# Performance work log

Measured on AMD Instinct MI355X. Metric: run time of the kernel, lower is better.

Reference implementation:

```python
import jax, jax.numpy as jnp
import numpy as np

ACT_BIT = 8
W_BIT = 8
EPS = 1e-8


def ste_round(x):
    # straight-through round (matches torch STE quant autograd)
    return x + jax.lax.stop_gradient(jnp.round(x) - x)


def quant_act(x):
    """Per-tensor symmetric 8-bit activation quantization (HAWQ QuantAct)."""
    n = 2 ** (ACT_BIT - 1) - 1  # 127
    x_max = jax.lax.stop_gradient(jnp.max(jnp.abs(x)))
    scale = jnp.maximum(x_max, EPS) / n
    x_int = jnp.clip(ste_round(x / scale), -n - 1, n)
    return x_int * scale, scale


def quant_linear(x_q, act_scale, weight, bias):
    """Per-channel symmetric 8-bit weight quant + integer matmul + fused dequant."""
    n = 2 ** (W_BIT - 1) - 1  # 127
    w_max = jax.lax.stop_gradient(jnp.max(jnp.abs(weight), axis=1, keepdims=True))  # [out,1]
    w_scale = jnp.maximum(w_max, EPS) / n                                            # [out,1]
    w_int = jnp.clip(ste_round(weight / w_scale), -n - 1, n)                         # [out,in]
    bias_scale = w_scale[:, 0] * act_scale                                           # [out]
    b_int = ste_round(bias / bias_scale)                                             # [out]
    x_int = x_q / act_scale                                   # integer-valued float, [..., in]
    out_int = jnp.einsum('...i,oi->...o', x_int, w_int)       # int8-domain GEMM in float
    return (out_int + b_int) * bias_scale                     # fused dequant


def setup_inputs() -> dict:
    key = jax.random.key(0)
    k1, k2, k3 = jax.random.split(key, 3)
    L, B, Q, D, O = 6, 8, 1024, 1024, 1024
    hs = jax.random.normal(k1, (L, B, Q, D), dtype=jnp.float32)
    weight = jax.random.normal(k2, (O, D), dtype=jnp.float32) * 0.02
    bias = jax.random.normal(k3, (O,), dtype=jnp.float32) * 0.02
    return {"hs": hs, "weight": weight, "bias": bias}


def reference(hs, weight, bias):
    x_q, act_scale = quant_act(hs)
    return quant_linear(x_q, act_scale, weight, bias)
```

## Files before the change

### kernel.cpp

```cpp
#include <hip/hip_runtime.h>
#include <stdint.h>

typedef int i32x4 __attribute__((ext_vector_type(4)));

#define K_DIM 1024
#define BM 256
#define BN 256
#define BKK 64
#define NKT (K_DIM / BKK)

__device__ __forceinline__ int quant1(float v, float inv) {
  float t = rintf(v * inv);
  t = fminf(fmaxf(t, -128.0f), 127.0f);
  return (int)t;
}

__device__ __forceinline__ void gld_lds16(const signed char* g, signed char* l) {
  typedef const __attribute__((address_space(1))) unsigned int* gp_t;
  typedef __attribute__((address_space(3))) unsigned int* lp_t;
  __builtin_amdgcn_global_load_lds((gp_t)(const void*)g, (lp_t)(void*)l, 16, 0, 0);
}

__global__ void absmax_kernel(const float* __restrict__ x, unsigned int* __restrict__ amax,
                              long long n4) {
  long long i = (long long)blockIdx.x * blockDim.x + threadIdx.x;
  const long long stride = (long long)gridDim.x * blockDim.x;
  const float4* x4 = (const float4*)x;
  float m = 0.0f;
  for (; i < n4; i += stride) {
    float4 v = x4[i];
    m = fmaxf(m, fmaxf(fmaxf(fabsf(v.x), fabsf(v.y)), fmaxf(fabsf(v.z), fabsf(v.w))));
  }
#pragma unroll
  for (int off = 32; off > 0; off >>= 1) m = fmaxf(m, __shfl_down(m, off, 64));
  __shared__ float sm[4];
  const int lane = threadIdx.x & 63, wid = threadIdx.x >> 6;
  if (lane == 0) sm[wid] = m;
  __syncthreads();
  if (threadIdx.x == 0) {
    float b = fmaxf(fmaxf(sm[0], sm[1]), fmaxf(sm[2], sm[3]));
    atomicMax(amax, __float_as_uint(b));
  }
}

__global__ void wquant_kernel(const float* __restrict__ w, const float* __restrict__ bias,
                              const unsigned int* __restrict__ amax_u,
                              signed char* __restrict__ wq,
                              float* __restrict__ bscale, float* __restrict__ bint) {
  const int o = blockIdx.x;
  const int t = threadIdx.x;
  float4 v = ((const float4*)(w + (size_t)o * K_DIM))[t];
  float m = fmaxf(fmaxf(fabsf(v.x), fabsf(v.y)), fmaxf(fabsf(v.z), fabsf(v.w)));
#pragma unroll
  for (int off = 32; off > 0; off >>= 1) m = fmaxf(m, __shfl_down(m, off, 64));
  __shared__ float sm[4];
  __shared__ float s_scale;
  const int lane = t & 63, wid = t >> 6;
  if (lane == 0) sm[wid] = m;
  __syncthreads();
  if (t == 0) {
    float wm = fmaxf(fmaxf(sm[0], sm[1]), fmaxf(sm[2], sm[3]));
    float wsc = fmaxf(wm, 1e-8f) / 127.0f;
    float asc = fmaxf(__uint_as_float(*amax_u), 1e-8f) / 127.0f;
    float bsc = wsc * asc;
    bscale[o] = bsc;
    bint[o] = rintf(bias[o] / bsc);
    s_scale = wsc;
  }
  __syncthreads();
  const float inv = 1.0f / s_scale;
  int q0 = quant1(v.x, inv), q1 = quant1(v.y, inv), q2 = quant1(v.z, inv), q3 = quant1(v.w, inv);
  unsigned int p = (unsigned)(q0 & 255) | ((unsigned)(q1 & 255) << 8) |
                   ((unsigned)(q2 & 255) << 16) | ((unsigned)(q3 & 255) << 24);
  ((unsigned int*)wq)[o * 256 + t] = p;
}

__global__ void aquant_kernel(const float* __restrict__ x, const unsigned int* __restrict__ amax_u,
                              unsigned int* __restrict__ q4, long long n4) {
  const float asc = fmaxf(__uint_as_float(*amax_u), 1e-8f) / 127.0f;
  const float inv = 1.0f / asc;
  long long i = (long long)blockIdx.x * blockDim.x + threadIdx.x;
  const long long stride = (long long)gridDim.x * blockDim.x;
  const float4* x4 = (const float4*)x;
  for (; i < n4; i += stride) {
    float4 v = x4[i];
    int q0 = quant1(v.x, inv), q1 = quant1(v.y, inv), q2 = quant1(v.z, inv), q3 = quant1(v.w, inv);
    q4[i] = (unsigned)(q0 & 255) | ((unsigned)(q1 & 255) << 8) |
            ((unsigned)(q2 & 255) << 16) | ((unsigned)(q3 & 255) << 24);
  }
}

__global__ __launch_bounds__(512, 2) void gemm_kernel(
    const signed char* __restrict__ A, const signed char* __restrict__ W,
    const float* __restrict__ bscale, const float* __restrict__ bint,
    float* __restrict__ out, int M, int N, int K) {
  extern __shared__ __align__(16) signed char smem[];
  signed char* Abase = smem;
  signed char* Bbase = smem + 65536;

  const int nwg = gridDim.x;
  const int orig = blockIdx.x;
  const int wgid = (orig & 7) * (nwg >> 3) + (orig >> 3);
  const int nbn = N / BN;
  const int bm = wgid / nbn;
  const int bn = wgid % nbn;
  const int m0 = bm * BM, n0 = bn * BN;

  const int tid = threadIdx.x;
  const int lane = tid & 63;
  const int wid = tid >> 6;
  const int wr = wid >> 2;
  const int wc = wid & 3;

  const int fr = lane & 15;
  const int fk = (lane >> 4) << 4;

  const signed char* ga = A + (size_t)(m0 + wid * 16 + fr) * K + fk;
  const signed char* gb = W + (size_t)(n0 + wid * 16 + fr) * K + fk;
  const size_t rs = (size_t)128 * K;

  i32x4 acc[8][4];
#pragma unroll
  for (int i = 0; i < 8; i++)
#pragma unroll
    for (int j = 0; j < 4; j++) acc[i][j] = (i32x4){0, 0, 0, 0};

  i32x4 af[4], bf[4];

#define SB __builtin_amdgcn_sched_barrier(0)
#define BAR __builtin_amdgcn_s_barrier()
#define WAIT_LGKM0 asm volatile("s_waitcnt lgkmcnt(0)" ::: "memory")

#define ISSUE_TILE(t)                                                     \
  do {                                                                    \
    const int b_ = (t) & 3;                                               \
    const int kof_ = (t) * BKK;                                           \
    gld_lds16(ga + kof_,      Abase + ((b_ * 16 + wid) << 10));           \
    gld_lds16(ga + kof_ + rs, Abase + ((b_ * 16 + wid + 8) << 10));       \
    gld_lds16(gb + kof_,      Bbase + ((b_ * 16 + wid) << 10));           \
    gld_lds16(gb + kof_ + rs, Bbase + ((b_ * 16 + wid + 8) << 10));       \
  } while (0)

#define RD_A(i_, mf_) af[i_] = *(const i32x4*)(Abase + (((buf_ * 16) + (mf_)) << 10) + lane * 16)
#define RD_B(j_, nf_) bf[j_] = *(const i32x4*)(Bbase + (((buf_ * 16) + (nf_)) << 10) + lane * 16)

#define MFMA8(IB, JB)                                                          \
  do {                                                                         \
    __builtin_amdgcn_s_setprio(1);                                             \
    _Pragma("unroll") for (int i_ = 0; i_ < 4; i_++)                           \
      _Pragma("unroll") for (int j_ = 0; j_ < 2; j_++)                         \
        acc[(IB) + i_][(JB) + j_] = __builtin_amdgcn_mfma_i32_16x16x64_i8(     \
            af[i_], bf[(JB) + j_], acc[(IB) + i_][(JB) + j_], 0, 0, 0);        \
    __builtin_amdgcn_s_setprio(0);                                             \
  } while (0)

#define TILE(t, DO_ISSUE, VMWAIT)                                              \
  do {                                                                         \
    const int buf_ = (t) & 3;                                                  \
                                                                  \
    RD_A(0, wr * 8 + 0); RD_A(1, wr * 8 + 1);                                  \
    RD_A(2, wr * 8 + 2); RD_A(3, wr * 8 + 3);                                  \
    RD_B(0, wc * 4 + 0); RD_B(1, wc * 4 + 1);                                  \
    if (DO_ISSUE) ISSUE_TILE((t) + 3);                                         \
    SB; BAR; SB; WAIT_LGKM0; SB;                                               \
    MFMA8(0, 0);                                                               \
    SB; BAR;                                                                   \
                                                                  \
    RD_B(2, wc * 4 + 2); RD_B(3, wc * 4 + 3);                                  \
    SB; BAR; SB; WAIT_LGKM0; SB;                                               \
    MFMA8(0, 2);                                                               \
    SB; BAR;                                                                   \
                                                                  \
    RD_A(0, wr * 8 + 4); RD_A(1, wr * 8 + 5);                                  \
    RD_A(2, wr * 8 + 6); RD_A(3, wr * 8 + 7);                                  \
    SB; BAR; SB; WAIT_LGKM0; SB;                                               \
    MFMA8(4, 2);                                                               \
    SB; BAR;                                                                   \
     \
    asm volatile("s_waitcnt " VMWAIT ::: "memory");                            \
    SB; BAR; SB;                                                               \
    MFMA8(4, 0);                                                               \
    SB; BAR;                                                                   \
  } while (0)

  ISSUE_TILE(0);
  ISSUE_TILE(1);
  ISSUE_TILE(2);
  asm volatile("s_waitcnt vmcnt(8)" ::: "memory");
  SB; BAR; SB;

#pragma unroll 1
  for (int t = 0; t < NKT - 3; ++t) {
    TILE(t, 1, "vmcnt(8)");
  }
  TILE(NKT - 3, 0, "vmcnt(4)");
  TILE(NKT - 2, 0, "vmcnt(0)");
  TILE(NKT - 1, 0, "vmcnt(0)");

#undef TILE
#undef MFMA8
#undef RD_A
#undef RD_B
#undef ISSUE_TILE

  float* Cst = (float*)smem;
  const int rr = (lane >> 4) * 4;
  const int cc = lane & 15;
#pragma unroll
  for (int h = 0; h < 2; ++h) {
    if (wr == h) {
#pragma unroll
      for (int j = 0; j < 4; j++) {
        const int colL = wc * 64 + j * 16 + cc;
        const float bs = bscale[n0 + colL];
        const float bi = bint[n0 + colL];
#pragma unroll
        for (int i = 0; i < 8; i++)
#pragma unroll
          for (int r = 0; r < 4; r++)
            Cst[(i * 16 + rr + r) * 256 + colL] = ((float)acc[i][j][r] + bi) * bs;
      }
    }
    WAIT_LGKM0;
    BAR;
    const size_t rowbase = (size_t)(m0 + h * 128) * N + n0;
#pragma unroll
    for (int it = 0; it < 16; ++it) {
      const int r_ = it * 8 + wid;
      float4 v = *(const float4*)&Cst[r_ * 256 + lane * 4];
      *(float4*)&out[rowbase + (size_t)r_ * N + lane * 4] = v;
    }
    WAIT_LGKM0;
    BAR;
  }
#undef WAIT_LGKM0
#undef BAR
#undef SB
}

extern "C" void kernel_launch(void* const* d_in, const int* in_sizes, int n_in,
                              void* d_out, int out_size, void* d_ws, size_t ws_size,
                              hipStream_t stream) {
  const float* hs = (const float*)d_in[0];
  const float* w = (const float*)d_in[1];
  const float* bias = (const float*)d_in[2];
  float* out = (float*)d_out;

  const long long n = (long long)in_sizes[0];
  const int K = K_DIM;
  const int O = in_sizes[2];
  const int M = (int)(n / K);

  char* ws = (char*)d_ws;
  unsigned int* amax_u = (unsigned int*)ws;
  float* bscale = (float*)(ws + 256);
  float* bint = (float*)(ws + 256 + 4096);
  signed char* wq = (signed char*)(ws + 65536);
  signed char* xq = (signed char*)(ws + 65536 + 1048576);

  hipFuncSetAttribute((const void*)gemm_kernel,
                      hipFuncAttributeMaxDynamicSharedMemorySize, 131072);

  hipMemsetAsync(amax_u, 0, 4, stream);

  const long long n4 = n / 4;
  absmax_kernel<<<2048, 256, 0, stream>>>(hs, amax_u, n4);
  wquant_kernel<<<O, 256, 0, stream>>>(w, bias, amax_u, wq, bscale, bint);
  aquant_kernel<<<2048, 256, 0, stream>>>(hs, amax_u, (unsigned int*)xq, n4);

  const int nblocks = (M / BM) * (O / BN);
  gemm_kernel<<<nblocks, 512, 131072, stream>>>(xq, wq, bscale, bint, out, M, O, K);
}
```

Baseline: 204.7 us.

## Pre-pack quantized A and W into MFMA fragment-tiled layout for contiguous loads

The activation and weight quantization kernels now write int8 data in a fragment-blocked layout (16-row by 64-k tiles of 1 KB, lane-ordered). The GEMM's direct-to-LDS loads become fully contiguous 1 KB chunks instead of strided 16-byte row segments. This targets better global-load coalescing and fewer DRAM pages touched per tile. In exchange, the aquant kernel now reads the float input with a strided gather pattern, which may hurt its bandwidth.

```diff
diff --git a/kernel.cpp b/kernel.cpp
--- a/kernel.cpp
+++ b/kernel.cpp
@@ -8,6 +8,7 @@
 #define BN 256
 #define BKK 64
 #define NKT (K_DIM / BKK)
+
 
 __device__ __forceinline__ int quant1(float v, float inv) {
   float t = rintf(v * inv);
@@ -72,21 +73,31 @@
   int q0 = quant1(v.x, inv), q1 = quant1(v.y, inv), q2 = quant1(v.z, inv), q3 = quant1(v.w, inv);
   unsigned int p = (unsigned)(q0 & 255) | ((unsigned)(q1 & 255) << 8) |
                    ((unsigned)(q2 & 255) << 16) | ((unsigned)(q3 & 255) << 24);
-  ((unsigned int*)wq)[o * 256 + t] = p;
+  const int F = o >> 4, T = t >> 4;
+  const int l = (((t >> 2) & 3) << 4) | (o & 15);
+  const int j = (t << 2) & 15;
+  *(unsigned int*)(wq + (((size_t)F << 14) + (T << 10) + (l << 4) + j)) = p;
 }
 
 __global__ void aquant_kernel(const float* __restrict__ x, const unsigned int* __restrict__ amax_u,
-                              unsigned int* __restrict__ q4, long long n4) {
+                              uint4* __restrict__ q16, int nchunk) {
   const float asc = fmaxf(__uint_as_float(*amax_u), 1e-8f) / 127.0f;
   const float inv = 1.0f / asc;
-  long long i = (long long)blockIdx.x * blockDim.x + threadIdx.x;
-  const long long stride = (long long)gridDim.x * blockDim.x;
-  const float4* x4 = (const float4*)x;
-  for (; i < n4; i += stride) {
-    float4 v = x4[i];
-    int q0 = quant1(v.x, inv), q1 = quant1(v.y, inv), q2 = quant1(v.z, inv), q3 = quant1(v.w, inv);
-    q4[i] = (unsigned)(q0 & 255) | ((unsigned)(q1 & 255) << 8) |
-            ((unsigned)(q2 & 255) << 16) | ((unsigned)(q3 & 255) << 24);
+  int c = blockIdx.x * blockDim.x + threadIdx.x;
+  const int stride = gridDim.x * blockDim.x;
+  for (; c < nchunk; c += stride) {
+    const int l = c & 63, T = (c >> 6) & 15, F = c >> 10;
+    const size_t src = (((size_t)(F << 4) + (l & 15)) << 10) + (T << 6) + ((l >> 4) << 4);
+    const float4* s4 = (const float4*)(x + src);
+    unsigned int r[4];
+#pragma unroll
+    for (int q = 0; q < 4; q++) {
+      float4 v = s4[q];
+      int q0 = quant1(v.x, inv), q1 = quant1(v.y, inv), q2 = quant1(v.z, inv), q3 = quant1(v.w, inv);
+      r[q] = (unsigned)(q0 & 255) | ((unsigned)(q1 & 255) << 8) |
+             ((unsigned)(q2 & 255) << 16) | ((unsigned)(q3 & 255) << 24);
+    }
+    q16[c] = make_uint4(r[0], r[1], r[2], r[3]);
   }
 }
 
@@ -112,12 +123,9 @@
   const int wr = wid >> 2;
   const int wc = wid & 3;
 
-  const int fr = lane & 15;
-  const int fk = (lane >> 4) << 4;
-
-  const signed char* ga = A + (size_t)(m0 + wid * 16 + fr) * K + fk;
-  const signed char* gb = W + (size_t)(n0 + wid * 16 + fr) * K + fk;
-  const size_t rs = (size_t)128 * K;
+  const signed char* gaf = A + (((size_t)(m0 >> 4) + wid) << 14) + (lane << 4);
+  const signed char* gbf = W + (((size_t)(n0 >> 4) + wid) << 14) + (lane << 4);
+  const size_t fs8 = (size_t)8 << 14;
 
   i32x4 acc[8][4];
 #pragma unroll
@@ -134,11 +142,11 @@
 #define ISSUE_TILE(t)                                                     \
   do {                                                                    \
     const int b_ = (t) & 3;                                               \
-    const int kof_ = (t) * BKK;                                           \
-    gld_lds16(ga + kof_,      Abase + ((b_ * 16 + wid) << 10));           \
-    gld_lds16(ga + kof_ + rs, Abase + ((b_ * 16 + wid + 8) << 10));       \
-    gld_lds16(gb + kof_,      Bbase + ((b_ * 16 + wid) << 10));           \
-    gld_lds16(gb + kof_ + rs, Bbase + ((b_ * 16 + wid + 8) << 10));       \
+    const int kof_ = (t) << 10;                                           \
+    gld_lds16(gaf + kof_,       Abase + ((b_ * 16 + wid) << 10));         \
+    gld_lds16(gaf + fs8 + kof_, Abase + ((b_ * 16 + wid + 8) << 10));     \
+    gld_lds16(gbf + kof_,       Bbase + ((b_ * 16 + wid) << 10));         \
+    gld_lds16(gbf + fs8 + kof_, Bbase + ((b_ * 16 + wid + 8) << 10));     \
   } while (0)
 
 #define RD_A(i_, mf_) af[i_] = *(const i32x4*)(Abase + (((buf_ * 16) + (mf_)) << 10) + lane * 16)
@@ -266,7 +274,8 @@
   const long long n4 = n / 4;
   absmax_kernel<<<2048, 256, 0, stream>>>(hs, amax_u, n4);
   wquant_kernel<<<O, 256, 0, stream>>>(w, bias, amax_u, wq, bscale, bint);
-  aquant_kernel<<<2048, 256, 0, stream>>>(hs, amax_u, (unsigned int*)xq, n4);
+  const int nchunk = (int)(n / 16);
+  aquant_kernel<<<2048, 256, 0, stream>>>(hs, amax_u, (uint4*)xq, nchunk);
 
   const int nblocks = (M / BM) * (O / BN);
   gemm_kernel<<<nblocks, 512, 131072, stream>>>(xq, wq, bscale, bint, out, M, O, K);
```

After: 189.7 us. 7.3% less time.
